# Optimization experiments

Measured on AMD Instinct MI355X. Metric: run time of the kernel, lower is better.

The kernel has to match this reference:

```python
import jax, jax.numpy as jnp
import numpy as np

D_MODEL = 1024
N_HEAD = 16
N_KV = 8
HEAD_DIM = D_MODEL // N_HEAD  # 64
ROPE_BASE = 10000.0


def _rope_tables(T, head_dim):
    inv_freq = 1.0 / (ROPE_BASE ** (jnp.arange(0, head_dim, 2, dtype=jnp.float32) / head_dim))
    pos = jnp.arange(T, dtype=jnp.float32)
    freqs = pos[:, None] * inv_freq[None, :]  # [T, head_dim//2]
    return jnp.sin(freqs), jnp.cos(freqs)


def _apply_rope(x, sin, cos):
    # x: [B, H, T, D]; sin/cos: [T, D//2] broadcast over B,H
    x1 = x[..., ::2]
    x2 = x[..., 1::2]
    y1 = x1 * cos - x2 * sin
    y2 = x1 * sin + x2 * cos
    return jnp.stack([y1, y2], axis=-1).reshape(x.shape)


def setup_inputs() -> dict:
    key = jax.random.key(0)
    ks = jax.random.split(key, 5)
    B, T = 2, 2048
    x = jax.random.normal(ks[0], (B, T, D_MODEL), dtype=jnp.float32)
    std = 0.02
    Wq = std * jax.random.normal(ks[1], (D_MODEL, D_MODEL), dtype=jnp.float32)
    Wk = std * jax.random.normal(ks[2], (N_KV * HEAD_DIM, D_MODEL), dtype=jnp.float32)
    Wv = std * jax.random.normal(ks[3], (N_KV * HEAD_DIM, D_MODEL), dtype=jnp.float32)
    Wo = std * jax.random.normal(ks[4], (D_MODEL, D_MODEL), dtype=jnp.float32)
    return {"x": x, "Wq": Wq, "Wk": Wk, "Wv": Wv, "Wo": Wo}


def reference(x, Wq, Wk, Wv, Wo):
    B, T, _ = x.shape
    G = N_HEAD // N_KV  # query heads per kv head (repeat_interleave grouping)

    # projections (bias-free Linear: x @ W.T)
    q = (x @ Wq.T).reshape(B, T, N_HEAD, HEAD_DIM).transpose(0, 2, 1, 3)  # [B,H,T,D]
    k = (x @ Wk.T).reshape(B, T, N_KV, HEAD_DIM).transpose(0, 2, 1, 3)   # [B,Hkv,T,D]
    v = (x @ Wv.T).reshape(B, T, N_KV, HEAD_DIM).transpose(0, 2, 1, 3)

    sin, cos = _rope_tables(T, HEAD_DIM)
    q = _apply_rope(q, sin, cos)
    k = _apply_rope(k, sin, cos)

    # GQA without materializing repeated K/V: group q heads by kv head.
    # repeat_interleave(dim=1) maps q head h -> kv head h // G.
    qg = q.reshape(B, N_KV, G, T, HEAD_DIM)
    scale = 1.0 / np.sqrt(HEAD_DIM)
    scores = jnp.einsum('bkgtd,bksd->bkgts', qg, k) * scale  # [B,Hkv,G,T,T]
    causal = jnp.tril(jnp.ones((T, T), dtype=bool))
    scores = jnp.where(causal, scores, jnp.float32(-1e30))
    attn = jax.nn.softmax(scores, axis=-1)
    y = jnp.einsum('bkgts,bksd->bkgtd', attn, v)              # [B,Hkv,G,T,D]
    y = y.reshape(B, N_HEAD, T, HEAD_DIM).transpose(0, 2, 1, 3).reshape(B, T, D_MODEL)
    return y @ Wo.T
```

## Files before the change

### kernel.cpp

```cpp
#include <hip/hip_runtime.h>
#include <cstdint>
#include <cstddef>

typedef __attribute__((ext_vector_type(8))) __bf16 bf16x8;
typedef __attribute__((ext_vector_type(4))) __bf16 bf16x4;
typedef __attribute__((ext_vector_type(4))) float f32x4;

#define DEVI __device__ __forceinline__

DEVI void gload_lds16(const void* g, void* l) {
    __builtin_amdgcn_global_load_lds((const __attribute__((address_space(1))) void*)g,
                                     (__attribute__((address_space(3))) void*)l, 16, 0, 0);
}

__global__ __launch_bounds__(256) void cvt_all(
    const float* __restrict__ x, const float* __restrict__ wq,
    const float* __restrict__ wk, const float* __restrict__ wv,
    const float* __restrict__ wo,
    bf16x4* __restrict__ xb, bf16x4* __restrict__ wqb, bf16x4* __restrict__ wkb,
    bf16x4* __restrict__ wvb, bf16x4* __restrict__ wob)
{
    int i = blockIdx.x * 256 + threadIdx.x;
    const int stride = gridDim.x * 256;
    for (; i < 1835008; i += stride) {
        const float4* s; bf16x4* d; int j;
        if (i < 1048576)      { s = (const float4*)x;  d = xb;  j = i; }
        else if (i < 1310720) { s = (const float4*)wq; d = wqb; j = i - 1048576; }
        else if (i < 1441792) { s = (const float4*)wk; d = wkb; j = i - 1310720; }
        else if (i < 1572864) { s = (const float4*)wv; d = wvb; j = i - 1441792; }
        else                  { s = (const float4*)wo; d = wob; j = i - 1572864; }
        float4 v = s[j];
        bf16x4 o = { (__bf16)v.x, (__bf16)v.y, (__bf16)v.z, (__bf16)v.w };
        d[j] = o;
    }
}

__global__ __launch_bounds__(256) void rope_tables(float* __restrict__ sint, float* __restrict__ cost)
{
    int i = blockIdx.x * 256 + threadIdx.x;
    int t = i >> 5, p = i & 31;
    float inv = powf(10000.0f, -(float)p / 32.0f);
    float f = (float)t * inv;
    float s, c;
    sincosf(f, &s, &c);
    sint[i] = s;
    cost[i] = c;
}

__global__ __launch_bounds__(256) void qkv_gemm(
    const __bf16* __restrict__ xb, const __bf16* __restrict__ wqb,
    const __bf16* __restrict__ wkb, const __bf16* __restrict__ wvb,
    const float* __restrict__ sint, const float* __restrict__ cost,
    __bf16* __restrict__ Qo, __bf16* __restrict__ Ko, __bf16* __restrict__ Vo)
{
    __shared__ __bf16 As[8192];
    __shared__ __bf16 Bs[8192];
    const int tid = threadIdx.x;
    const int lane = tid & 63;
    const int wid = tid >> 6;
    const int wm = (wid >> 1) * 64, wn = (wid & 1) * 64;
    const int m0 = blockIdx.y * 128;
    const int n0 = blockIdx.x * 128;

    const __bf16* bsrc;
    if (n0 < 1024)      bsrc = wqb + (size_t)n0 * 1024;
    else if (n0 < 1536) bsrc = wkb + (size_t)(n0 - 1024) * 1024;
    else                bsrc = wvb + (size_t)(n0 - 1536) * 1024;
    const __bf16* asrc = xb + (size_t)m0 * 1024;

    f32x4 acc[4][4] = {};
    const int srow = tid >> 3, schunk = tid & 7;

    for (int k0 = 0; k0 < 1024; k0 += 64) {
        __syncthreads();
#pragma unroll
        for (int it = 0; it < 4; ++it) {
            int r = srow + it * 32;
            int gc = (schunk ^ (r & 7)) * 8;
            gload_lds16(asrc + (size_t)r * 1024 + k0 + gc, (char*)As + r * 128 + schunk * 16);
            gload_lds16(bsrc + (size_t)r * 1024 + k0 + gc, (char*)Bs + r * 128 + schunk * 16);
        }
        __syncthreads();
#pragma unroll
        for (int ks = 0; ks < 2; ++ks) {
            bf16x8 af[4], bfv[4];
#pragma unroll
            for (int i = 0; i < 4; ++i) {
                int ra = wm + i * 16 + (lane & 15);
                af[i] = *(const bf16x8*)((const char*)As + ra * 128 + (((ks * 4 + (lane >> 4)) ^ (ra & 7)) * 16));
                int rb = wn + i * 16 + (lane & 15);
                bfv[i] = *(const bf16x8*)((const char*)Bs + rb * 128 + (((ks * 4 + (lane >> 4)) ^ (rb & 7)) * 16));
            }
#pragma unroll
            for (int mi = 0; mi < 4; ++mi)
#pragma unroll
                for (int ni = 0; ni < 4; ++ni)
                    acc[mi][ni] = __builtin_amdgcn_mfma_f32_16x16x32_bf16(af[mi], bfv[ni], acc[mi][ni], 0, 0, 0);
        }
    }

    const int rg = lane >> 4, cf = lane & 15;
#pragma unroll
    for (int mi = 0; mi < 4; ++mi) {
#pragma unroll
        for (int ni = 0; ni < 4; ++ni) {
#pragma unroll
            for (int r = 0; r < 4; ++r) {
                float v = acc[mi][ni][r];
                float pv = __shfl_xor(v, 1, 64);
                int m = m0 + wm + mi * 16 + rg * 4 + r;
                int n = n0 + wn + ni * 16 + cf;
                int b = m >> 11;
                int t = m & 2047;
                if (n < 1024) {
                    int h = n >> 6, d = n & 63;
                    float s = sint[t * 32 + (d >> 1)], c = cost[t * 32 + (d >> 1)];
                    float o = (d & 1) ? (pv * s + v * c) : (v * c - pv * s);
                    Qo[((size_t)(b * 16 + h) * 2048 + t) * 64 + d] = (__bf16)(o * 0.125f);
                } else if (n < 1536) {
                    int nn = n - 1024;
                    int h = nn >> 6, d = nn & 63;
                    float s = sint[t * 32 + (d >> 1)], c = cost[t * 32 + (d >> 1)];
                    float o = (d & 1) ? (pv * s + v * c) : (v * c - pv * s);
                    Ko[((size_t)(b * 8 + h) * 2048 + t) * 64 + d] = (__bf16)o;
                } else {
                    int nn = n - 1536;
                    int h = nn >> 6, d = nn & 63;
                    Vo[((size_t)(b * 8 + h) * 2048 + t) * 64 + d] = (__bf16)v;
                }
            }
        }
    }
}

__global__ __launch_bounds__(256) void v_transpose(const __bf16* __restrict__ Vg, __bf16* __restrict__ VTg)
{
    __shared__ __bf16 tile[64][72];
    const int tid = threadIdx.x;
    const int t0 = blockIdx.x * 64;
    const int bh = blockIdx.y;
    const size_t base = (size_t)bh * 2048 * 64;
    const int rr = tid >> 3, c8 = (tid & 7) * 8;
#pragma unroll
    for (int it = 0; it < 2; ++it) {
        int tt = rr + it * 32;
        *(bf16x8*)(&tile[tt][c8]) = *(const bf16x8*)(Vg + base + (size_t)(t0 + tt) * 64 + c8);
    }
    __syncthreads();
#pragma unroll
    for (int it = 0; it < 2; ++it) {
        int d = rr + it * 32;
        bf16x8 o;
#pragma unroll
        for (int j = 0; j < 8; ++j) o[j] = tile[c8 + j][d];
        *(bf16x8*)(VTg + base + (size_t)d * 2048 + t0 + c8) = o;
    }
}

__global__ __launch_bounds__(256, 2) void attn_fwd(
    const __bf16* __restrict__ Qg, const __bf16* __restrict__ Kg,
    const __bf16* __restrict__ VTg, __bf16* __restrict__ Yg)
{
    __shared__ char Ks[2][8192];
    __shared__ char Vs[2][8192];
    __shared__ char Pl[8192];
    const int tid = threadIdx.x;
    const int lane = tid & 63;
    const int w = tid >> 6;
    const int lin = blockIdx.x;
    const int xcd = lin & 7, g = (lin >> 3) & 3, p = lin >> 5;
    const int bh = xcd + 8 * g;
    const int b = bh >> 4, h = bh & 15, kvh = h >> 1;
    const size_t qbase = (size_t)(b * 16 + h) * 2048 * 64;
    const size_t kbase = (size_t)(b * 8 + kvh) * 2048 * 64;
    const int rg = lane >> 4, cf = lane & 15;
    char* pw = Pl + w * 2048;

    const int sr = tid >> 3;
    const int sc = tid & 7;
    const int gsc = (sc ^ (sr & 7)) * 8;

    const int Ja = p, Jb = 31 - p;
    bf16x8 pk0, pk1, pv0, pv1;

    bf16x8 ones;
#pragma unroll
    for (int e = 0; e < 8; ++e) ones[e] = (__bf16)1.0f;

#define PRE(NT) do {                                                                    \
    const int _n0 = (NT) * 64;                                                          \
    pk0 = *(const bf16x8*)(Kg + kbase + (size_t)(_n0 + sr) * 64 + gsc);                 \
    pk1 = *(const bf16x8*)(Kg + kbase + (size_t)(_n0 + sr + 32) * 64 + gsc);            \
    pv0 = *(const bf16x8*)(VTg + kbase + (size_t)sr * 2048 + _n0 + gsc);                \
    pv1 = *(const bf16x8*)(VTg + kbase + (size_t)(sr + 32) * 2048 + _n0 + gsc);         \
} while (0)
#define WRITE_LDS(BUF) do {                                                             \
    *(bf16x8*)(Ks[BUF] + tid * 16) = pk0;                                               \
    *(bf16x8*)(Ks[BUF] + (tid + 256) * 16) = pk1;                                       \
    *(bf16x8*)(Vs[BUF] + tid * 16) = pv0;                                               \
    *(bf16x8*)(Vs[BUF] + (tid + 256) * 16) = pv1;                                       \
} while (0)

    PRE(0);
    WRITE_LDS(0);
    __syncthreads();

    bf16x8 qf[2];
    f32x4 oacc[4], lacc;
    int J = Ja, nt = 0, cur = 0;

#pragma unroll 1
    for (int s = 0; s <= 32; ++s) {
        const int r0 = J * 64 + w * 16;
        if (nt == 0) {
#pragma unroll
            for (int ks = 0; ks < 2; ++ks)
                qf[ks] = *(const bf16x8*)(Qg + qbase + (size_t)(r0 + cf) * 64 + ks * 32 + rg * 8);
#pragma unroll
            for (int r = 0; r < 4; ++r) oacc[r] = f32x4{};
            lacc = f32x4{};
        }

        if (s < 32) {
            const int nnt = (nt == J) ? 0 : nt + 1;
            PRE(nnt);
        }

        {
            bf16x8 kf[2][4];
#pragma unroll
            for (int ks = 0; ks < 2; ++ks)
#pragma unroll
                for (int ni = 0; ni < 4; ++ni)
                    kf[ks][ni] = *(const bf16x8*)(Ks[cur] + (ni * 16 + cf) * 128 + (((ks * 4 + rg) ^ (cf & 7)) * 16));

            f32x4 sacc[4] = {};
            __builtin_amdgcn_s_setprio(1);
#pragma unroll
            for (int ks = 0; ks < 2; ++ks)
#pragma unroll
                for (int ni = 0; ni < 4; ++ni)
                    sacc[ni] = __builtin_amdgcn_mfma_f32_16x16x32_bf16(qf[ks], kf[ks][ni], sacc[ni], 0, 0, 0);
            __builtin_amdgcn_s_setprio(0);

            bf16x8 vf[2][4];
#pragma unroll
            for (int ks = 0; ks < 2; ++ks)
#pragma unroll
                for (int df = 0; df < 4; ++df)
                    vf[ks][df] = *(const bf16x8*)(Vs[cur] + (df * 16 + cf) * 128 + (((ks * 4 + rg) ^ (cf & 7)) * 16));

            if (nt == J) {
#pragma unroll
                for (int ni = 0; ni < 4; ++ni)
#pragma unroll
                    for (int r = 0; r < 4; ++r)
                        if (ni * 16 + cf > w * 16 + rg * 4 + r)
                            sacc[ni][r] = -3.0e38f;
            }

#pragma unroll
            for (int ni = 0; ni < 4; ++ni)
#pragma unroll
                for (int r = 0; r < 4; ++r)
                    sacc[ni][r] = __expf(sacc[ni][r]);

#pragma unroll
            for (int ni = 0; ni < 4; ++ni)
#pragma unroll
                for (int r = 0; r < 4; ++r) {
                    int pr = rg * 4 + r;
                    int pc = ni * 16 + cf;
                    *(__bf16*)(pw + pr * 128 + (((pc >> 3) ^ (pr & 7)) * 8 + (pc & 7)) * 2) =
                        (__bf16)sacc[ni][r];
                }

            __builtin_amdgcn_s_setprio(1);
#pragma unroll
            for (int ks = 0; ks < 2; ++ks) {
                bf16x8 pf = *(const bf16x8*)(pw + cf * 128 + (((ks * 4 + rg) ^ (cf & 7)) * 16));
#pragma unroll
                for (int df = 0; df < 4; ++df)
                    oacc[df] = __builtin_amdgcn_mfma_f32_16x16x32_bf16(pf, vf[ks][df], oacc[df], 0, 0, 0);
                lacc = __builtin_amdgcn_mfma_f32_16x16x32_bf16(pf, ones, lacc, 0, 0, 0);
            }
            __builtin_amdgcn_s_setprio(0);
        }

        if (nt == J) {
#pragma unroll
            for (int r = 0; r < 4; ++r) {
                float inv = 1.0f / lacc[r];
                int t = r0 + rg * 4 + r;
#pragma unroll
                for (int df = 0; df < 4; ++df)
                    Yg[((size_t)b * 2048 + t) * 1024 + h * 64 + df * 16 + cf] =
                        (__bf16)(oacc[df][r] * inv);
            }
        }

        if (s < 32) WRITE_LDS(cur ^ 1);
        __syncthreads();
        cur ^= 1;
        if (nt == J) { J = Jb; nt = 0; } else ++nt;
    }
#undef PRE
#undef WRITE_LDS
}

__global__ __launch_bounds__(256) void out_gemm(
    const __bf16* __restrict__ Yb, const __bf16* __restrict__ Wob, float* __restrict__ outp)
{
    __shared__ __bf16 As[8192];
    __shared__ __bf16 Bs[8192];
    const int tid = threadIdx.x;
    const int lane = tid & 63;
    const int wid = tid >> 6;
    const int wm = (wid >> 1) * 64, wn = (wid & 1) * 64;
    const int m0 = blockIdx.y * 128;
    const int n0 = blockIdx.x * 128;
    const __bf16* asrc = Yb + (size_t)m0 * 1024;
    const __bf16* bsrc = Wob + (size_t)n0 * 1024;

    f32x4 acc[4][4] = {};
    const int srow = tid >> 3, schunk = tid & 7;

    for (int k0 = 0; k0 < 1024; k0 += 64) {
        __syncthreads();
#pragma unroll
        for (int it = 0; it < 4; ++it) {
            int r = srow + it * 32;
            int gc = (schunk ^ (r & 7)) * 8;
            gload_lds16(asrc + (size_t)r * 1024 + k0 + gc, (char*)As + r * 128 + schunk * 16);
            gload_lds16(bsrc + (size_t)r * 1024 + k0 + gc, (char*)Bs + r * 128 + schunk * 16);
        }
        __syncthreads();
#pragma unroll
        for (int ks = 0; ks < 2; ++ks) {
            bf16x8 af[4], bfv[4];
#pragma unroll
            for (int i = 0; i < 4; ++i) {
                int ra = wm + i * 16 + (lane & 15);
                af[i] = *(const bf16x8*)((const char*)As + ra * 128 + (((ks * 4 + (lane >> 4)) ^ (ra & 7)) * 16));
                int rb = wn + i * 16 + (lane & 15);
                bfv[i] = *(const bf16x8*)((const char*)Bs + rb * 128 + (((ks * 4 + (lane >> 4)) ^ (rb & 7)) * 16));
            }
#pragma unroll
            for (int mi = 0; mi < 4; ++mi)
#pragma unroll
                for (int ni = 0; ni < 4; ++ni)
                    acc[mi][ni] = __builtin_amdgcn_mfma_f32_16x16x32_bf16(af[mi], bfv[ni], acc[mi][ni], 0, 0, 0);
        }
    }

    const int rg = lane >> 4, cf = lane & 15;
#pragma unroll
    for (int mi = 0; mi < 4; ++mi)
#pragma unroll
        for (int ni = 0; ni < 4; ++ni)
#pragma unroll
            for (int r = 0; r < 4; ++r) {
                int m = m0 + wm + mi * 16 + rg * 4 + r;
                int n = n0 + wn + ni * 16 + cf;
                outp[(size_t)m * 1024 + n] = acc[mi][ni][r];
            }
}

extern "C" void kernel_launch(void* const* d_in, const int* in_sizes, int n_in,
                              void* d_out, int out_size, void* d_ws, size_t ws_size,
                              hipStream_t stream)
{
    const float* x  = (const float*)d_in[0];
    const float* wq = (const float*)d_in[1];
    const float* wk = (const float*)d_in[2];
    const float* wv = (const float*)d_in[3];
    const float* wo = (const float*)d_in[4];

    char* ws = (char*)d_ws;
    __bf16* xb  = (__bf16*)(ws + 0);
    __bf16* wqb = (__bf16*)(ws + 8388608);
    __bf16* wkb = (__bf16*)(ws + 10485760);
    __bf16* wvb = (__bf16*)(ws + 11534336);
    __bf16* wob = (__bf16*)(ws + 12582912);
    __bf16* Qb  = (__bf16*)(ws + 14680064);
    __bf16* Kb  = (__bf16*)(ws + 23068672);
    __bf16* Vb  = (__bf16*)(ws + 27262976);
    __bf16* VTb = (__bf16*)(ws + 31457280);
    __bf16* Yb  = (__bf16*)(ws + 35651584);
    float* sint = (float*)(ws + 44040192);
    float* cost = (float*)(ws + 44302336);
    if (ws_size < 44564480) return;

    cvt_all<<<2048, 256, 0, stream>>>(x, wq, wk, wv, wo,
                                      (bf16x4*)xb, (bf16x4*)wqb, (bf16x4*)wkb,
                                      (bf16x4*)wvb, (bf16x4*)wob);
    rope_tables<<<256, 256, 0, stream>>>(sint, cost);
    qkv_gemm<<<dim3(16, 32), 256, 0, stream>>>(xb, wqb, wkb, wvb, sint, cost, Qb, Kb, Vb);
    v_transpose<<<dim3(32, 16), 256, 0, stream>>>(Vb, VTb);
    attn_fwd<<<512, 256, 0, stream>>>(Qb, Kb, VTb, Yb);
    out_gemm<<<dim3(8, 32), 256, 0, stream>>>(Yb, wob, (float*)d_out);
}
```

Baseline: 114.6 us.

## Double-buffer LDS in QKV and output GEMMs; shrink output tile to 128x64

Both GEMMs now use two LDS buffers and prefetch the next K-slice with global_load_lds while computing on the current one, leaving one barrier per iteration instead of two. The output GEMM tile shrinks from 128x128 to 128x64, with each wave owning 32 rows, which doubles the grid to 512 blocks for better CU coverage. LDS use per block doubles in qkv_gemm, which may lower occupancy, and the smaller out_gemm tile reloads A more often.

```diff
diff --git a/kernel.cpp b/kernel.cpp
--- a/kernel.cpp
+++ b/kernel.cpp
@@ -53,8 +53,8 @@
     const float* __restrict__ sint, const float* __restrict__ cost,
     __bf16* __restrict__ Qo, __bf16* __restrict__ Ko, __bf16* __restrict__ Vo)
 {
-    __shared__ __bf16 As[8192];
-    __shared__ __bf16 Bs[8192];
+    __shared__ __bf16 As[2][8192];
+    __shared__ __bf16 Bs[2][8192];
     const int tid = threadIdx.x;
     const int lane = tid & 63;
     const int wid = tid >> 6;
@@ -70,26 +70,32 @@
 
     f32x4 acc[4][4] = {};
     const int srow = tid >> 3, schunk = tid & 7;
-
-    for (int k0 = 0; k0 < 1024; k0 += 64) {
-        __syncthreads();
-#pragma unroll
-        for (int it = 0; it < 4; ++it) {
-            int r = srow + it * 32;
-            int gc = (schunk ^ (r & 7)) * 8;
-            gload_lds16(asrc + (size_t)r * 1024 + k0 + gc, (char*)As + r * 128 + schunk * 16);
-            gload_lds16(bsrc + (size_t)r * 1024 + k0 + gc, (char*)Bs + r * 128 + schunk * 16);
-        }
-        __syncthreads();
+    const int gc = (schunk ^ (srow & 7)) * 8;
+
+#define STAGE(BUF, K0) do {                                                             \
+    _Pragma("unroll") for (int it = 0; it < 4; ++it) {                                  \
+        int r = srow + it * 32;                                                         \
+        gload_lds16(asrc + (size_t)r * 1024 + (K0) + gc, (char*)As[BUF] + r * 128 + schunk * 16); \
+        gload_lds16(bsrc + (size_t)r * 1024 + (K0) + gc, (char*)Bs[BUF] + r * 128 + schunk * 16); \
+    }                                                                                   \
+} while (0)
+
+    STAGE(0, 0);
+    __syncthreads();
+
+#pragma unroll 1
+    for (int step = 0; step < 16; ++step) {
+        const int cur = step & 1;
+        if (step < 15) STAGE(cur ^ 1, (step + 1) * 64);
 #pragma unroll
         for (int ks = 0; ks < 2; ++ks) {
             bf16x8 af[4], bfv[4];
 #pragma unroll
             for (int i = 0; i < 4; ++i) {
                 int ra = wm + i * 16 + (lane & 15);
-                af[i] = *(const bf16x8*)((const char*)As + ra * 128 + (((ks * 4 + (lane >> 4)) ^ (ra & 7)) * 16));
+                af[i] = *(const bf16x8*)((const char*)As[cur] + ra * 128 + (((ks * 4 + (lane >> 4)) ^ (ra & 7)) * 16));
                 int rb = wn + i * 16 + (lane & 15);
-                bfv[i] = *(const bf16x8*)((const char*)Bs + rb * 128 + (((ks * 4 + (lane >> 4)) ^ (rb & 7)) * 16));
+                bfv[i] = *(const bf16x8*)((const char*)Bs[cur] + rb * 128 + (((ks * 4 + (lane >> 4)) ^ (rb & 7)) * 16));
             }
 #pragma unroll
             for (int mi = 0; mi < 4; ++mi)
@@ -97,7 +103,9 @@
                 for (int ni = 0; ni < 4; ++ni)
                     acc[mi][ni] = __builtin_amdgcn_mfma_f32_16x16x32_bf16(af[mi], bfv[ni], acc[mi][ni], 0, 0, 0);
         }
-    }
+        __syncthreads();
+    }
+#undef STAGE
 
     const int rg = lane >> 4, cf = lane & 15;
 #pragma unroll
@@ -311,57 +319,71 @@
 __global__ __launch_bounds__(256) void out_gemm(
     const __bf16* __restrict__ Yb, const __bf16* __restrict__ Wob, float* __restrict__ outp)
 {
-    __shared__ __bf16 As[8192];
-    __shared__ __bf16 Bs[8192];
+    __shared__ __bf16 As[2][8192];
+    __shared__ __bf16 Bs[2][4096];
     const int tid = threadIdx.x;
     const int lane = tid & 63;
     const int wid = tid >> 6;
-    const int wm = (wid >> 1) * 64, wn = (wid & 1) * 64;
+    const int wm = wid * 32;
     const int m0 = blockIdx.y * 128;
-    const int n0 = blockIdx.x * 128;
+    const int n0 = blockIdx.x * 64;
     const __bf16* asrc = Yb + (size_t)m0 * 1024;
     const __bf16* bsrc = Wob + (size_t)n0 * 1024;
 
-    f32x4 acc[4][4] = {};
+    f32x4 acc[2][4] = {};
     const int srow = tid >> 3, schunk = tid & 7;
-
-    for (int k0 = 0; k0 < 1024; k0 += 64) {
-        __syncthreads();
-#pragma unroll
-        for (int it = 0; it < 4; ++it) {
-            int r = srow + it * 32;
-            int gc = (schunk ^ (r & 7)) * 8;
-            gload_lds16(asrc + (size_t)r * 1024 + k0 + gc, (char*)As + r * 128 + schunk * 16);
-            gload_lds16(bsrc + (size_t)r * 1024 + k0 + gc, (char*)Bs + r * 128 + schunk * 16);
-        }
-        __syncthreads();
+    const int gc = (schunk ^ (srow & 7)) * 8;
+
+#define STAGE(BUF, K0) do {                                                             \
+    _Pragma("unroll") for (int it = 0; it < 4; ++it) {                                  \
+        int r = srow + it * 32;                                                         \
+        gload_lds16(asrc + (size_t)r * 1024 + (K0) + gc, (char*)As[BUF] + r * 128 + schunk * 16); \
+    }                                                                                   \
+    _Pragma("unroll") for (int it = 0; it < 2; ++it) {                                  \
+        int r = srow + it * 32;                                                         \
+        gload_lds16(bsrc + (size_t)r * 1024 + (K0) + gc, (char*)Bs[BUF] + r * 128 + schunk * 16); \
+    }                                                                                   \
+} while (0)
+
+    STAGE(0, 0);
+    __syncthreads();
+
+#pragma unroll 1
+    for (int step = 0; step < 16; ++step) {
+        const int cur = step & 1;
+        if (step < 15) STAGE(cur ^ 1, (step + 1) * 64);
 #pragma unroll
         for (int ks = 0; ks < 2; ++ks) {
-            bf16x8 af[4], bfv[4];
+            bf16x8 af[2], bfv[4];
+#pragma unroll
+            for (int i = 0; i < 2; ++i) {
+                int ra = wm + i * 16 + (lane & 15);
+                af[i] = *(const bf16x8*)((const char*)As[cur] + ra * 128 + (((ks * 4 + (lane >> 4)) ^ (ra & 7)) * 16));
+            }
 #pragma unroll
             for (int i = 0; i < 4; ++i) {
-                int ra = wm + i * 16 + (lane & 15);
-                af[i] = *(const bf16x8*)((const char*)As + ra * 128 + (((ks * 4 + (lane >> 4)) ^ (ra & 7)) * 16));
-                int rb = wn + i * 16 + (lane & 15);
-                bfv[i] = *(const bf16x8*)((const char*)Bs + rb * 128 + (((ks * 4 + (lane >> 4)) ^ (rb & 7)) * 16));
-            }
-#pragma unroll
-            for (int mi = 0; mi < 4; ++mi)
+                int rb = i * 16 + (lane & 15);
+                bfv[i] = *(const bf16x8*)((const char*)Bs[cur] + rb * 128 + (((ks * 4 + (lane >> 4)) ^ (rb & 7)) * 16));
+            }
+#pragma unroll
+            for (int mi = 0; mi < 2; ++mi)
 #pragma unroll
                 for (int ni = 0; ni < 4; ++ni)
                     acc[mi][ni] = __builtin_amdgcn_mfma_f32_16x16x32_bf16(af[mi], bfv[ni], acc[mi][ni], 0, 0, 0);
         }
-    }
+        __syncthreads();
+    }
+#undef STAGE
 
     const int rg = lane >> 4, cf = lane & 15;
 #pragma unroll
-    for (int mi = 0; mi < 4; ++mi)
+    for (int mi = 0; mi < 2; ++mi)
 #pragma unroll
         for (int ni = 0; ni < 4; ++ni)
 #pragma unroll
             for (int r = 0; r < 4; ++r) {
                 int m = m0 + wm + mi * 16 + rg * 4 + r;
-                int n = n0 + wn + ni * 16 + cf;
+                int n = n0 + ni * 16 + cf;
                 outp[(size_t)m * 1024 + n] = acc[mi][ni][r];
             }
 }
@@ -398,5 +420,5 @@
     qkv_gemm<<<dim3(16, 32), 256, 0, stream>>>(xb, wqb, wkb, wvb, sint, cost, Qb, Kb, Vb);
     v_transpose<<<dim3(32, 16), 256, 0, stream>>>(Vb, VTb);
     attn_fwd<<<512, 256, 0, stream>>>(Qb, Kb, VTb, Yb);
-    out_gemm<<<dim3(8, 32), 256, 0, stream>>>(Yb, wob, (float*)d_out);
-}
+    out_gemm<<<dim3(16, 32), 256, 0, stream>>>(Yb, wob, (float*)d_out);
+}
```

New measurement: 106.0 us. 7.5% less time.
